# Performance work log

Measured on AMD Instinct MI355X. Metric: run time of the kernel, lower is better.

Reference implementation:

```python
import jax, jax.numpy as jnp
import numpy as np

MAX_M = 16


def _twiddle(n, m):
    # exp(-2i*pi*n_a*m_a / (n*m)), shape (n, m), precomputed on host (static n, m)
    a = np.outer(np.arange(n), np.arange(m))
    return jnp.asarray(np.exp(-2j * np.pi * a / (n * m)).astype(np.complex64))


def _ref_dft_real(n, H):
    # reference DFT matrix as (H, n, n, 2) real view, matching ref_dft_matrix
    a = np.outer(np.arange(n), np.arange(n))
    M = np.exp(-2j * np.pi * a / n).astype(np.complex64)  # (n, n)
    M = np.broadcast_to(M, (H, n, n))
    return jnp.asarray(np.stack([M.real, M.imag], axis=-1).astype(np.float32))


def _cooley_tukey(k, n, m, mats):
    # k: (..., H, n*m) complex; mats[p]: (H, p, p) complex
    k = k.reshape(*k.shape[:-1], m, n)                      # (..., H, m, n)
    kf = jnp.einsum('hmo,...hon->...hmn', mats[m], k)       # m-length DFTs
    kf = jnp.einsum('nm,...mn->...nm', _twiddle(n, m), kf)  # twiddle + transpose -> (..., H, n, m)
    if n <= MAX_M:
        kf = jnp.einsum('hno,...hom->...hnm', mats[n], kf)  # n-length DFTs
    else:
        kf = jnp.moveaxis(kf, -1, -3)                        # '... h n m -> ... m h n'
        kf = _cooley_tukey(kf, n // MAX_M, MAX_M, mats)
        kf = jnp.moveaxis(kf, -3, -1)                        # '... m h n -> ... h n m'
    return kf.reshape(*kf.shape[:-2], n * m)


def block_fft(x, N, mats):
    # x: (..., H, L) complex, zero-pad to N, then recursive block FFT
    L = x.shape[-1]
    if L != N:
        x = jnp.pad(x, [(0, 0)] * (x.ndim - 1) + [(0, N - L)])
    return _cooley_tukey(x, N // MAX_M, MAX_M, mats)


def block_ifft(x, N, mats):
    return jnp.conj(block_fft(jnp.conj(x), N, mats)) / N


def setup_inputs() -> dict:
    key = jax.random.key(0)
    B, H, L = 16, 512, 1024
    ku, kk, kd = jax.random.split(key, 3)
    u = jax.random.normal(ku, (B, H, L), dtype=jnp.float32)
    k = jax.random.normal(kk, (H, L), dtype=jnp.float32) / L
    D = jax.random.normal(kd, (H,), dtype=jnp.float32)
    return {
        'u': u, 'k': k, 'D': D,
        'mat_2': _ref_dft_real(2, H),
        'mat_4': _ref_dft_real(4, H),
        'mat_8': _ref_dft_real(8, H),
        'mat_16': _ref_dft_real(16, H),
    }


def reference(u, k, D, mat_2, mat_4, mat_8, mat_16):
    cplx = lambda m: (m[..., 0] + 1j * m[..., 1]).astype(jnp.complex64)
    mats = {2: cplx(mat_2), 4: cplx(mat_4), 8: cplx(mat_8), 16: cplx(mat_16)}
    L = u.shape[-1]
    N = 2 * L  # causal FFT conv length
    k_f = block_fft(k.astype(jnp.complex64), N, mats)   # (H, N)
    u_f = block_fft(u.astype(jnp.complex64), N, mats)   # (B, H, N)
    y = block_ifft(u_f * k_f, N, mats)[..., :L].real    # (B, H, L)
    return (y + u * D[:, None]).astype(jnp.float32)
```

## Files before the change

kernel.cpp:

```cpp
#include <hip/hip_runtime.h>
#include <math.h>

#define NT     128
#define NB     16
#define NH     512
#define SEQ_L  1024
#define FFT_N  2048
#define RS     0.70710678118654752f
#define C16    0.92387953251128675f
#define S16    0.38268343236508977f

#define P(x) ((x) + ((x) >> 4))
#define BUF_SZ 2176

__device__ __align__(16) float2 g_kf[(size_t)NH * FFT_N];

__device__ __forceinline__ float2 cmul(float2 a, float2 b) {
    return make_float2(a.x * b.x - a.y * b.y, a.x * b.y + a.y * b.x);
}
__device__ __forceinline__ float2 cmulj(float2 a, float2 b) {
    return make_float2(a.x * b.x + a.y * b.y, a.y * b.x - a.x * b.y);
}
__device__ __forceinline__ float2 cadd(float2 a, float2 b) { return make_float2(a.x + b.x, a.y + b.y); }
__device__ __forceinline__ float2 csub(float2 a, float2 b) { return make_float2(a.x - b.x, a.y - b.y); }

template <int SIGN>
__device__ __forceinline__ void dft4(float2 x[4]) {
    float2 s0 = cadd(x[0], x[2]), s1 = csub(x[0], x[2]);
    float2 s2 = cadd(x[1], x[3]), s3 = csub(x[1], x[3]);
    x[0] = cadd(s0, s2);
    x[2] = csub(s0, s2);
    if (SIGN < 0) {
        x[1] = make_float2(s1.x + s3.y, s1.y - s3.x);
        x[3] = make_float2(s1.x - s3.y, s1.y + s3.x);
    } else {
        x[1] = make_float2(s1.x - s3.y, s1.y + s3.x);
        x[3] = make_float2(s1.x + s3.y, s1.y - s3.x);
    }
}

template <int SIGN>
__device__ __forceinline__ void dft8(float2 x[8]) {
    float2 e0 = cadd(x[0], x[4]), e1 = cadd(x[1], x[5]);
    float2 e2 = cadd(x[2], x[6]), e3 = cadd(x[3], x[7]);
    float2 o0 = csub(x[0], x[4]), o1 = csub(x[1], x[5]);
    float2 o2 = csub(x[2], x[6]), o3 = csub(x[3], x[7]);
    float2 t1, t2, t3;
    if (SIGN < 0) {
        t1 = make_float2(RS * (o1.x + o1.y), RS * (o1.y - o1.x));
        t2 = make_float2(o2.y, -o2.x);
        t3 = make_float2(-RS * (o3.x - o3.y), -RS * (o3.x + o3.y));
    } else {
        t1 = make_float2(RS * (o1.x - o1.y), RS * (o1.x + o1.y));
        t2 = make_float2(-o2.y, o2.x);
        t3 = make_float2(RS * (-o3.x - o3.y), RS * (o3.x - o3.y));
    }
    float2 s0 = cadd(e0, e2), s1 = csub(e0, e2), s2 = cadd(e1, e3), s3 = csub(e1, e3);
    x[0] = cadd(s0, s2);
    x[4] = csub(s0, s2);
    float2 u0 = cadd(o0, t2), u1 = csub(o0, t2), u2 = cadd(t1, t3), u3 = csub(t1, t3);
    x[1] = cadd(u0, u2);
    x[5] = csub(u0, u2);
    if (SIGN < 0) {
        x[2] = make_float2(s1.x + s3.y, s1.y - s3.x);
        x[6] = make_float2(s1.x - s3.y, s1.y + s3.x);
        x[3] = make_float2(u1.x + u3.y, u1.y - u3.x);
        x[7] = make_float2(u1.x - u3.y, u1.y + u3.x);
    } else {
        x[2] = make_float2(s1.x - s3.y, s1.y + s3.x);
        x[6] = make_float2(s1.x + s3.y, s1.y - s3.x);
        x[3] = make_float2(u1.x - u3.y, u1.y + u3.x);
        x[7] = make_float2(u1.x + u3.y, u1.y - u3.x);
    }
}

template <int SIGN>
__device__ __forceinline__ void dft16_twiddle(float2 v[4][4]) {
    const float sg = (SIGN < 0) ? -1.f : 1.f;
    const float2 W1 = make_float2(C16, sg * S16);
    const float2 W2 = make_float2(RS, sg * RS);
    const float2 W3 = make_float2(S16, sg * C16);
    const float2 W6 = make_float2(-RS, sg * RS);
    const float2 W9 = make_float2(-C16, -sg * S16);
    v[1][1] = cmul(v[1][1], W1);
    v[1][2] = cmul(v[1][2], W2);
    v[1][3] = cmul(v[1][3], W3);
    v[2][1] = cmul(v[2][1], W2);
    v[2][2] = make_float2(-sg * v[2][2].y, sg * v[2][2].x);
    v[2][3] = cmul(v[2][3], W6);
    v[3][1] = cmul(v[3][1], W3);
    v[3][2] = cmul(v[3][2], W6);
    v[3][3] = cmul(v[3][3], W9);
}

template <int SIGN>
__device__ __forceinline__ void dft16(float2 x[16]) {
    float2 v[4][4];
#pragma unroll
    for (int n0 = 0; n0 < 4; ++n0) {
        float2 a[4] = {x[n0], x[n0 + 4], x[n0 + 8], x[n0 + 12]};
        dft4<SIGN>(a);
        v[n0][0] = a[0]; v[n0][1] = a[1]; v[n0][2] = a[2]; v[n0][3] = a[3];
    }
    dft16_twiddle<SIGN>(v);
#pragma unroll
    for (int k0 = 0; k0 < 4; ++k0) {
        float2 a[4] = {v[0][k0], v[1][k0], v[2][k0], v[3][k0]};
        dft4<SIGN>(a);
        x[k0] = a[0]; x[k0 + 4] = a[1]; x[k0 + 8] = a[2]; x[k0 + 12] = a[3];
    }
}

__device__ __forceinline__ void dft16_zero8(const float2 z[8], float2 x[16]) {
    float2 v[4][4];
#pragma unroll
    for (int n0 = 0; n0 < 4; ++n0) {
        float2 a = z[n0], b = z[n0 + 4];
        v[n0][0] = cadd(a, b);
        v[n0][1] = make_float2(a.x + b.y, a.y - b.x);
        v[n0][2] = csub(a, b);
        v[n0][3] = make_float2(a.x - b.y, a.y + b.x);
    }
    dft16_twiddle<-1>(v);
#pragma unroll
    for (int k0 = 0; k0 < 4; ++k0) {
        float2 a[4] = {v[0][k0], v[1][k0], v[2][k0], v[3][k0]};
        dft4<-1>(a);
        x[k0] = a[0]; x[k0 + 4] = a[1]; x[k0 + 8] = a[2]; x[k0 + 12] = a[3];
    }
}

__device__ __forceinline__ void dft16_inv_low8(const float2 x[16], float2 y[8]) {
    float2 v[4][4];
#pragma unroll
    for (int n0 = 0; n0 < 4; ++n0) {
        float2 a[4] = {x[n0], x[n0 + 4], x[n0 + 8], x[n0 + 12]};
        dft4<+1>(a);
        v[n0][0] = a[0]; v[n0][1] = a[1]; v[n0][2] = a[2]; v[n0][3] = a[3];
    }
    dft16_twiddle<+1>(v);
#pragma unroll
    for (int k0 = 0; k0 < 4; ++k0) {
        float2 x0 = v[0][k0], x1 = v[1][k0], x2 = v[2][k0], x3 = v[3][k0];
        float2 s0 = cadd(x0, x2), s1 = csub(x0, x2);
        float2 s2 = cadd(x1, x3), s3 = csub(x1, x3);
        y[k0]     = cadd(s0, s2);
        y[k0 + 4] = make_float2(s1.x - s3.y, s1.y + s3.x);
    }
}

template <int CONJ>
__device__ __forceinline__ void tw_apply16(float2 x[16], float2 a) {
#define AP(v, w) (v) = CONJ ? cmulj((v), (w)) : cmul((v), (w))
    AP(x[1], a);
    float2 w2 = cmul(a, a);      AP(x[2], w2);
    float2 w3 = cmul(w2, a);     AP(x[3], w3);
    float2 w4 = cmul(w2, w2);    AP(x[4], w4);
    float2 w5 = cmul(w4, a);     AP(x[5], w5);
    float2 w6 = cmul(w4, w2);    AP(x[6], w6);
    float2 w7 = cmul(w6, a);     AP(x[7], w7);
    float2 w8 = cmul(w4, w4);    AP(x[8], w8);
    float2 w9 = cmul(w8, a);     AP(x[9], w9);
    float2 w10 = cmul(w8, w2);   AP(x[10], w10);
    float2 w11 = cmul(w10, a);   AP(x[11], w11);
    float2 w12 = cmul(w8, w4);   AP(x[12], w12);
    float2 w13 = cmul(w12, a);   AP(x[13], w13);
    float2 w14 = cmul(w12, w2);  AP(x[14], w14);
    float2 w15 = cmul(w14, a);   AP(x[15], w15);
#undef AP
}

__global__ __launch_bounds__(NT, 2) void kfft_kernel(const float* __restrict__ kin) {
    __shared__ float re[BUF_SZ];
    __shared__ float im[BUF_SZ];
    __shared__ float2 twlds[NT];
    const int t = threadIdx.x;
    const int h = blockIdx.x;
    float2 w1;
    {
        float sv, cv;
        sincosf(-6.283185307179586f * (float)t / (float)FFT_N, &sv, &cv);
        w1 = make_float2(cv, sv);
        twlds[t] = w1;
    }
    const float* krow = kin + (size_t)h * SEQ_L;
    {
        float2 z[8], x[16];
#pragma unroll
        for (int j = 0; j < 8; ++j) z[j] = make_float2(krow[t + 128 * j], 0.f);
        dft16_zero8(z, x);
        tw_apply16<0>(x, w1);
#pragma unroll
        for (int c = 0; c < 16; ++c) {
            const int id = P(t + 128 * c);
            re[id] = x[c].x; im[id] = x[c].y;
        }
    }
    __syncthreads();
    const int cblk = t >> 3, r = t & 7;
    const int base = 128 * cblk + r;
    {
        float2 x[16];
#pragma unroll
        for (int j = 0; j < 16; ++j) {
            const int id = P(base + 8 * j);
            x[j] = make_float2(re[id], im[id]);
        }
        dft16<-1>(x);
        tw_apply16<0>(x, twlds[16 * r]);
#pragma unroll
        for (int c2 = 0; c2 < 16; ++c2) {
            const int id = P(base + 8 * c2);
            re[id] = x[c2].x; im[id] = x[c2].y;
        }
    }
    __syncthreads();
#pragma unroll
    for (int gi = 0; gi < 2; ++gi) {
        const int g = 2 * t + gi;
        float2 x[8];
#pragma unroll
        for (int l = 0; l < 8; ++l) {
            const int id = P(8 * g + l);
            x[l] = make_float2(re[id], im[id]);
        }
        dft8<-1>(x);
        float4* o4 = (float4*)(g_kf + (size_t)h * FFT_N + 8 * g);
#pragma unroll
        for (int l = 0; l < 4; ++l)
            o4[l] = make_float4(x[2 * l].x, x[2 * l].y, x[2 * l + 1].x, x[2 * l + 1].y);
    }
}

__global__ __launch_bounds__(NT, 2) void conv_pair_kernel(const float* __restrict__ u,
                                                          const float* __restrict__ D,
                                                          float* __restrict__ out) {
    __shared__ float re[BUF_SZ];
    __shared__ float im[BUF_SZ];
    __shared__ float2 twlds[NT];
    const int t = threadIdx.x;
    const int h = blockIdx.x & (NH - 1);
    const int bp = blockIdx.x >> 9;
    const size_t row0 = (size_t)(2 * bp) * NH + h;
    const size_t row1 = row0 + NH;
    float2 w1;
    {
        float sv, cv;
        sincosf(-6.283185307179586f * (float)t / (float)FFT_N, &sv, &cv);
        w1 = make_float2(cv, sv);
        twlds[t] = w1;
    }
    const float* u0 = u + row0 * SEQ_L;
    const float* u1 = u + row1 * SEQ_L;
    {
        float2 z[8], x[16];
#pragma unroll
        for (int j = 0; j < 8; ++j)
            z[j] = make_float2(u0[t + 128 * j], u1[t + 128 * j]);
        dft16_zero8(z, x);
        tw_apply16<0>(x, w1);
#pragma unroll
        for (int c = 0; c < 16; ++c) {
            const int id = P(t + 128 * c);
            re[id] = x[c].x; im[id] = x[c].y;
        }
    }
    __syncthreads();
    const int cblk = t >> 3, r = t & 7;
    const int base = 128 * cblk + r;
    const float2 ws = twlds[16 * r];
    {
        float2 x[16];
#pragma unroll
        for (int j = 0; j < 16; ++j) {
            const int id = P(base + 8 * j);
            x[j] = make_float2(re[id], im[id]);
        }
        dft16<-1>(x);
        tw_apply16<0>(x, ws);
#pragma unroll
        for (int c2 = 0; c2 < 16; ++c2) {
            const int id = P(base + 8 * c2);
            re[id] = x[c2].x; im[id] = x[c2].y;
        }
    }
    __syncthreads();
    {
        const float2* kfr = g_kf + (size_t)h * FFT_N;
#pragma unroll
        for (int gi = 0; gi < 2; ++gi) {
            const int g = 2 * t + gi;
            float2 x[8];
#pragma unroll
            for (int l = 0; l < 8; ++l) {
                const int id = P(8 * g + l);
                x[l] = make_float2(re[id], im[id]);
            }
            dft8<-1>(x);
            const float4* k4 = (const float4*)(kfr + 8 * g);
#pragma unroll
            for (int l = 0; l < 4; ++l) {
                float4 kk = k4[l];
                x[2 * l]     = cmul(x[2 * l],     make_float2(kk.x, kk.y));
                x[2 * l + 1] = cmul(x[2 * l + 1], make_float2(kk.z, kk.w));
            }
            dft8<+1>(x);
#pragma unroll
            for (int l = 0; l < 8; ++l) {
                const int id = P(8 * g + l);
                re[id] = x[l].x; im[id] = x[l].y;
            }
        }
    }
    __syncthreads();
    float up0[8], up1[8];
#pragma unroll
    for (int j = 0; j < 8; ++j) {
        up0[j] = u0[t + 128 * j];
        up1[j] = u1[t + 128 * j];
    }
    {
        float2 x[16];
#pragma unroll
        for (int c2 = 0; c2 < 16; ++c2) {
            const int id = P(base + 8 * c2);
            x[c2] = make_float2(re[id], im[id]);
        }
        tw_apply16<1>(x, ws);
        dft16<+1>(x);
#pragma unroll
        for (int j = 0; j < 16; ++j) {
            const int id = P(base + 8 * j);
            re[id] = x[j].x; im[id] = x[j].y;
        }
    }
    __syncthreads();
    {
        float2 x[16];
#pragma unroll
        for (int c = 0; c < 16; ++c) {
            const int id = P(t + 128 * c);
            x[c] = make_float2(re[id], im[id]);
        }
        tw_apply16<1>(x, w1);
        float2 y[8];
        dft16_inv_low8(x, y);
        const float Dh = D[h];
        const float invN = 1.0f / (float)FFT_N;
        float* o0row = out + row0 * SEQ_L;
        float* o1row = out + row1 * SEQ_L;
#pragma unroll
        for (int j = 0; j < 8; ++j) {
            o0row[t + 128 * j] = y[j].x * invN + up0[j] * Dh;
            o1row[t + 128 * j] = y[j].y * invN + up1[j] * Dh;
        }
    }
}

extern "C" void kernel_launch(void* const* d_in, const int* in_sizes, int n_in,
                              void* d_out, int out_size, void* d_ws, size_t ws_size,
                              hipStream_t stream) {
    const float* u = (const float*)d_in[0];
    const float* k = (const float*)d_in[1];
    const float* D = (const float*)d_in[2];
    float* out = (float*)d_out;

    kfft_kernel<<<NH, NT, 0, stream>>>(k);
    conv_pair_kernel<<<NB * NH / 2, NT, 0, stream>>>(u, D, out);
}
```

Before: 113.5 us.

## Precompute twiddle tables, coalesce k-spectrum layout, simplify LDS indexing, raise occupancy

The k-FFT kernel now also writes global twiddle tables for both radix-16 stages, and the conv kernel loads them instead of calling sincos and building powers by repeated complex multiplies. The k spectrum is stored as float4 in a thread-strided layout, so each thread's loads are coalesced across the wavefront. LDS padded indices are computed from per-thread bases with constant offsets, and launch bounds request 4 blocks per SM. In exchange the conv kernel issues more global (cached) loads per stage, and the higher occupancy target may force register spills.

Measured after the change: 117.4 us. +3.4%, slower.

```diff
diff --git a/kernel.cpp b/kernel.cpp
--- a/kernel.cpp
+++ b/kernel.cpp
@@ -10,10 +10,11 @@
 #define C16    0.92387953251128675f
 #define S16    0.38268343236508977f
 
-#define P(x) ((x) + ((x) >> 4))
 #define BUF_SZ 2176
 
-__device__ __align__(16) float2 g_kf[(size_t)NH * FFT_N];
+__device__ __align__(16) float4 g_kf4[(size_t)NH * (FFT_N / 2)];
+__device__ float2 g_tw1[15 * 128];
+__device__ float2 g_tw2[15 * 8];
 
 __device__ __forceinline__ float2 cmul(float2 a, float2 b) {
     return make_float2(a.x * b.x - a.y * b.y, a.x * b.y + a.y * b.x);
@@ -176,6 +177,21 @@
     __shared__ float2 twlds[NT];
     const int t = threadIdx.x;
     const int h = blockIdx.x;
+    {
+        const int gid = h * NT + t;
+        if (gid < 15 * 128) {
+            const int c = (gid >> 7) + 1, tt = gid & 127;
+            float sv, cv;
+            sincosf(-6.283185307179586f * (float)(c * tt) / (float)FFT_N, &sv, &cv);
+            g_tw1[gid] = make_float2(cv, sv);
+        } else if (gid < 15 * 128 + 15 * 8) {
+            const int i2 = gid - 15 * 128;
+            const int c = (i2 >> 3) + 1, r = i2 & 7;
+            float sv, cv;
+            sincosf(-6.283185307179586f * (float)(c * r) / 128.f, &sv, &cv);
+            g_tw2[i2] = make_float2(cv, sv);
+        }
+    }
     float2 w1;
     {
         float sv, cv;
@@ -183,6 +199,7 @@
         w1 = make_float2(cv, sv);
         twlds[t] = w1;
     }
+    const int pb1 = t + (t >> 4);
     const float* krow = kin + (size_t)h * SEQ_L;
     {
         float2 z[8], x[16];
@@ -192,122 +209,118 @@
         tw_apply16<0>(x, w1);
 #pragma unroll
         for (int c = 0; c < 16; ++c) {
-            const int id = P(t + 128 * c);
+            const int id = pb1 + 136 * c;
             re[id] = x[c].x; im[id] = x[c].y;
         }
     }
     __syncthreads();
     const int cblk = t >> 3, r = t & 7;
-    const int base = 128 * cblk + r;
+    const int pb2 = 136 * cblk + r;
     {
         float2 x[16];
 #pragma unroll
         for (int j = 0; j < 16; ++j) {
-            const int id = P(base + 8 * j);
+            const int id = pb2 + 8 * j + (j >> 1);
             x[j] = make_float2(re[id], im[id]);
         }
         dft16<-1>(x);
         tw_apply16<0>(x, twlds[16 * r]);
 #pragma unroll
         for (int c2 = 0; c2 < 16; ++c2) {
-            const int id = P(base + 8 * c2);
+            const int id = pb2 + 8 * c2 + (c2 >> 1);
             re[id] = x[c2].x; im[id] = x[c2].y;
         }
     }
     __syncthreads();
+    const int pb3 = 17 * t;
+    float4* kf4 = g_kf4 + (size_t)h * (FFT_N / 2);
 #pragma unroll
     for (int gi = 0; gi < 2; ++gi) {
-        const int g = 2 * t + gi;
         float2 x[8];
 #pragma unroll
         for (int l = 0; l < 8; ++l) {
-            const int id = P(8 * g + l);
+            const int id = pb3 + 8 * gi + l;
             x[l] = make_float2(re[id], im[id]);
         }
         dft8<-1>(x);
-        float4* o4 = (float4*)(g_kf + (size_t)h * FFT_N + 8 * g);
-#pragma unroll
-        for (int l = 0; l < 4; ++l)
-            o4[l] = make_float4(x[2 * l].x, x[2 * l].y, x[2 * l + 1].x, x[2 * l + 1].y);
-    }
-}
-
-__global__ __launch_bounds__(NT, 2) void conv_pair_kernel(const float* __restrict__ u,
+#pragma unroll
+        for (int q = 0; q < 4; ++q)
+            kf4[(4 * gi + q) * 128 + t] =
+                make_float4(x[2 * q].x, x[2 * q].y, x[2 * q + 1].x, x[2 * q + 1].y);
+    }
+}
+
+__global__ __launch_bounds__(NT, 4) void conv_pair_kernel(const float* __restrict__ u,
                                                           const float* __restrict__ D,
                                                           float* __restrict__ out) {
     __shared__ float re[BUF_SZ];
     __shared__ float im[BUF_SZ];
-    __shared__ float2 twlds[NT];
     const int t = threadIdx.x;
     const int h = blockIdx.x & (NH - 1);
     const int bp = blockIdx.x >> 9;
     const size_t row0 = (size_t)(2 * bp) * NH + h;
     const size_t row1 = row0 + NH;
-    float2 w1;
-    {
-        float sv, cv;
-        sincosf(-6.283185307179586f * (float)t / (float)FFT_N, &sv, &cv);
-        w1 = make_float2(cv, sv);
-        twlds[t] = w1;
-    }
     const float* u0 = u + row0 * SEQ_L;
     const float* u1 = u + row1 * SEQ_L;
+    const int pb1 = t + (t >> 4);
     {
         float2 z[8], x[16];
 #pragma unroll
         for (int j = 0; j < 8; ++j)
             z[j] = make_float2(u0[t + 128 * j], u1[t + 128 * j]);
         dft16_zero8(z, x);
-        tw_apply16<0>(x, w1);
+#pragma unroll
+        for (int c = 1; c < 16; ++c)
+            x[c] = cmul(x[c], g_tw1[(c - 1) * 128 + t]);
 #pragma unroll
         for (int c = 0; c < 16; ++c) {
-            const int id = P(t + 128 * c);
+            const int id = pb1 + 136 * c;
             re[id] = x[c].x; im[id] = x[c].y;
         }
     }
     __syncthreads();
     const int cblk = t >> 3, r = t & 7;
-    const int base = 128 * cblk + r;
-    const float2 ws = twlds[16 * r];
+    const int pb2 = 136 * cblk + r;
     {
         float2 x[16];
 #pragma unroll
         for (int j = 0; j < 16; ++j) {
-            const int id = P(base + 8 * j);
+            const int id = pb2 + 8 * j + (j >> 1);
             x[j] = make_float2(re[id], im[id]);
         }
         dft16<-1>(x);
-        tw_apply16<0>(x, ws);
+#pragma unroll
+        for (int c = 1; c < 16; ++c)
+            x[c] = cmul(x[c], g_tw2[(c - 1) * 8 + r]);
 #pragma unroll
         for (int c2 = 0; c2 < 16; ++c2) {
-            const int id = P(base + 8 * c2);
+            const int id = pb2 + 8 * c2 + (c2 >> 1);
             re[id] = x[c2].x; im[id] = x[c2].y;
         }
     }
     __syncthreads();
     {
-        const float2* kfr = g_kf + (size_t)h * FFT_N;
+        const float4* kf4 = g_kf4 + (size_t)h * (FFT_N / 2);
+        const int pb3 = 17 * t;
 #pragma unroll
         for (int gi = 0; gi < 2; ++gi) {
-            const int g = 2 * t + gi;
             float2 x[8];
 #pragma unroll
             for (int l = 0; l < 8; ++l) {
-                const int id = P(8 * g + l);
+                const int id = pb3 + 8 * gi + l;
                 x[l] = make_float2(re[id], im[id]);
             }
             dft8<-1>(x);
-            const float4* k4 = (const float4*)(kfr + 8 * g);
-#pragma unroll
-            for (int l = 0; l < 4; ++l) {
-                float4 kk = k4[l];
-                x[2 * l]     = cmul(x[2 * l],     make_float2(kk.x, kk.y));
-                x[2 * l + 1] = cmul(x[2 * l + 1], make_float2(kk.z, kk.w));
+#pragma unroll
+            for (int q = 0; q < 4; ++q) {
+                float4 kk = kf4[(4 * gi + q) * 128 + t];
+                x[2 * q]     = cmul(x[2 * q],     make_float2(kk.x, kk.y));
+                x[2 * q + 1] = cmul(x[2 * q + 1], make_float2(kk.z, kk.w));
             }
             dft8<+1>(x);
 #pragma unroll
             for (int l = 0; l < 8; ++l) {
-                const int id = P(8 * g + l);
+                const int id = pb3 + 8 * gi + l;
                 re[id] = x[l].x; im[id] = x[l].y;
             }
         }
@@ -323,14 +336,16 @@
         float2 x[16];
 #pragma unroll
         for (int c2 = 0; c2 < 16; ++c2) {
-            const int id = P(base + 8 * c2);
+            const int id = pb2 + 8 * c2 + (c2 >> 1);
             x[c2] = make_float2(re[id], im[id]);
         }
-        tw_apply16<1>(x, ws);
+#pragma unroll
+        for (int c = 1; c < 16; ++c)
+            x[c] = cmulj(x[c], g_tw2[(c - 1) * 8 + r]);
         dft16<+1>(x);
 #pragma unroll
         for (int j = 0; j < 16; ++j) {
-            const int id = P(base + 8 * j);
+            const int id = pb2 + 8 * j + (j >> 1);
             re[id] = x[j].x; im[id] = x[j].y;
         }
     }
@@ -339,10 +354,12 @@
         float2 x[16];
 #pragma unroll
         for (int c = 0; c < 16; ++c) {
-            const int id = P(t + 128 * c);
+            const int id = pb1 + 136 * c;
             x[c] = make_float2(re[id], im[id]);
         }
-        tw_apply16<1>(x, w1);
+#pragma unroll
+        for (int c = 1; c < 16; ++c)
+            x[c] = cmulj(x[c], g_tw1[(c - 1) * 128 + t]);
         float2 y[8];
         dft16_inv_low8(x, y);
         const float Dh = D[h];
```
